# Performance work log

Hardware: AMD Instinct MI355X
Metric: run time of the kernel (lower is better)

## Reference

```python
import jax, jax.numpy as jnp
import numpy as np

B, S, E, H = 2, 2048, 1024, 16
D = E // H  # head_dim = 64


def setup_inputs() -> dict:
    key = jax.random.key(0)
    ks = jax.random.split(key, 6)
    scale = 1.0 / np.sqrt(E)
    query = jax.random.normal(ks[0], (B, S, E), dtype=jnp.float32)
    key_t = jax.random.normal(ks[1], (B, S, E), dtype=jnp.float32)
    # causal mask: True where future positions should be masked
    attention_mask = jnp.triu(jnp.ones((S, S), dtype=jnp.bool_), k=1)
    wq = jax.random.normal(ks[2], (E, E), dtype=jnp.float32) * scale
    wk = jax.random.normal(ks[3], (E, E), dtype=jnp.float32) * scale
    wv = jax.random.normal(ks[4], (E, E), dtype=jnp.float32) * scale
    wo = jax.random.normal(ks[5], (E, E), dtype=jnp.float32) * scale
    return {"query": query, "key": key_t, "attention_mask": attention_mask,
            "wq": wq, "wk": wk, "wv": wv, "wo": wo}


def _split_heads(x):
    # (B, S, E) -> (B, H, S, D)
    return x.reshape(B, S, H, D).transpose(0, 2, 1, 3)


def reference(query, key, attention_mask, wq, wk, wv, wo):
    # self-attention (encoder_decoder_attention=False): k, v from query
    q = _split_heads(query @ wq.T)
    k = _split_heads(query @ wk.T)
    v = _split_heads(query @ wv.T)
    scores = jnp.einsum('bhqd,bhkd->bhqk', q, k) / np.sqrt(D)
    # causal mask broadcast (1,1,S,S)
    scores = jnp.where(attention_mask[None, None, :, :], -jnp.inf, scores)
    attn_weights = jax.nn.softmax(scores, axis=-1)
    # drop_out = 0.0, so dropout is identity
    attn_out = jnp.einsum('bhqk,bhkd->bhqd', attn_weights, v)
    attn_out = attn_out.transpose(0, 2, 1, 3).reshape(B, S, E)
    attn_out = attn_out @ wo.T
    return attn_out, attn_weights
```

## Files before the change

kernel.cpp:

```cpp
#include <hip/hip_runtime.h>
#include <hip/hip_bf16.h>
#include <cstdint>

#define S_LEN 2048
#define EMB 1024
#define NHEAD 16
#define HDIM 64
#define NB 2
#define MTOT (NB * S_LEN)

typedef __attribute__((ext_vector_type(8))) __bf16 bf16x8;
typedef __attribute__((ext_vector_type(8))) unsigned short us8;
typedef __attribute__((ext_vector_type(4))) unsigned short us4;
typedef __attribute__((ext_vector_type(4))) float f32x4;

__device__ __forceinline__ unsigned short f2b(float f) {
  unsigned int u = __float_as_uint(f);
  u = (u + 0x7FFFu + ((u >> 16) & 1u)) >> 16;
  return (unsigned short)u;
}
__device__ __forceinline__ unsigned short f2b_tr(float f) {
  return (unsigned short)(__float_as_uint(f) >> 16);
}
__device__ __forceinline__ float b2f(unsigned short u) {
  return __uint_as_float((unsigned int)u << 16);
}
__device__ __forceinline__ bf16x8 ld8(const unsigned short* p) {
  return __builtin_bit_cast(bf16x8, *(const us8*)p);
}
__device__ __forceinline__ void gload16(const void* g, void* l) {
  __builtin_amdgcn_global_load_lds(
      (const __attribute__((address_space(1))) unsigned int*)g,
      (__attribute__((address_space(3))) unsigned int*)l, 16, 0, 0);
}
__device__ __forceinline__ void st_nt(float* p, f32x4 v) {
  __builtin_nontemporal_store(v, (f32x4*)p);
}
__device__ __forceinline__ void bar_lds() {
  asm volatile("s_waitcnt lgkmcnt(0)" ::: "memory");
  __builtin_amdgcn_sched_barrier(0);
  __builtin_amdgcn_s_barrier();
}
__device__ __forceinline__ void fence_lds_wave() {
  asm volatile("s_waitcnt lgkmcnt(0)" ::: "memory");
  __builtin_amdgcn_sched_barrier(0);
}

__global__ void conv_fused(const float* __restrict__ X,
                           const float* __restrict__ wq, const float* __restrict__ wk,
                           const float* __restrict__ wv, const float* __restrict__ wo,
                           unsigned short* __restrict__ xb,
                           unsigned short* __restrict__ wb) {
  int i = blockIdx.x * blockDim.x + threadIdx.x;
  const float* s;
  unsigned short* o;
  int j;
  float sc = 1.0f;
  if (i < MTOT * EMB / 4) {
    s = X; j = i; o = xb;
  } else {
    int k = i - MTOT * EMB / 4;
    int sel = k >> 18;
    j = k & 262143;
    s = sel == 0 ? wq : sel == 1 ? wk : sel == 2 ? wv : wo;
    o = wb + (size_t)sel * EMB * EMB;
    if (sel == 0) sc = 0.125f;
  }
  float4 v = reinterpret_cast<const float4*>(s)[j];
  us4 ov;
  ov[0] = f2b(v.x * sc); ov[1] = f2b(v.y * sc);
  ov[2] = f2b(v.z * sc); ov[3] = f2b(v.w * sc);
  reinterpret_cast<us4*>(o)[j] = ov;
}

__global__ __launch_bounds__(256)
void vtrans(const unsigned short* __restrict__ V, unsigned short* __restrict__ VT) {
  __shared__ unsigned short Vs[64][72];
  const int s0 = blockIdx.x * 64;
  const int bh = blockIdx.y, b = bh >> 4, h = bh & 15;
  const unsigned short* Vb = V + (size_t)b * S_LEN * EMB + h * HDIM;
  const int t = threadIdx.x;
  {
    int row = t >> 2, c0 = (t & 3) * 16;
    const unsigned short* src = Vb + (size_t)(s0 + row) * EMB + c0;
    *(us8*)&Vs[row][c0] = *(const us8*)src;
    *(us8*)&Vs[row][c0 + 8] = *(const us8*)(src + 8);
  }
  __syncthreads();
  int d = t >> 2, sc = (t & 3) * 16;
  us8 o0, o1;
#pragma unroll
  for (int j = 0; j < 8; ++j) { o0[j] = Vs[sc + j][d]; o1[j] = Vs[sc + 8 + j][d]; }
  unsigned short* dst = VT + ((size_t)bh * HDIM + d) * S_LEN + s0 + sc;
  *(us8*)dst = o0;
  *(us8*)(dst + 8) = o1;
}

template <typename OT>
__global__ __launch_bounds__(256)
void gemm_bt(const unsigned short* __restrict__ A,
             const unsigned short* __restrict__ Wb,
             OT* __restrict__ Cb) {
  __shared__ unsigned short As[128 * 32];
  __shared__ unsigned short Bs[128 * 32];
  const int t = threadIdx.x;
  const int w = t >> 6, l = t & 63;
  const int m0 = blockIdx.x * 128;
  const int n0g = blockIdx.y * 128;
  const int wsel = n0g >> 10;
  const int n0 = n0g & 1023;
  const unsigned short* W = Wb + (size_t)wsel * ((size_t)EMB * EMB);
  OT* C = Cb + (size_t)wsel * ((size_t)MTOT * EMB);
  const int wr = (w >> 1) * 64, wc = (w & 1) * 64;
  const int fr = l & 15, fk = (l >> 4) * 8;
  const f32x4 fz = {0.f, 0.f, 0.f, 0.f};
  f32x4 acc[4][4];
  for (int i = 0; i < 4; i++)
    for (int j = 0; j < 4; j++) acc[i][j] = fz;
  const int srow = t >> 2, scol = (t & 3) * 8;
  const unsigned short* Ar = A + (size_t)(m0 + srow) * EMB + scol;
  const unsigned short* Wr = W + (size_t)(n0 + srow) * EMB + scol;
  unsigned short* lA = &As[t * 8];
  unsigned short* lB = &Bs[t * 8];
  for (int k0 = 0; k0 < EMB; k0 += 32) {
    gload16(Ar + k0, lA);
    gload16(Ar + (size_t)64 * EMB + k0, lA + 64 * 32);
    gload16(Wr + k0, lB);
    gload16(Wr + (size_t)64 * EMB + k0, lB + 64 * 32);
    __syncthreads();
    bf16x8 af[4], bg[4];
#pragma unroll
    for (int i = 0; i < 4; i++) {
      af[i] = ld8(&As[(wr + i * 16 + fr) * 32 + fk]);
      bg[i] = ld8(&Bs[(wc + i * 16 + fr) * 32 + fk]);
    }
#pragma unroll
    for (int i = 0; i < 4; i++)
#pragma unroll
      for (int j = 0; j < 4; j++)
        acc[i][j] = __builtin_amdgcn_mfma_f32_16x16x32_bf16(af[i], bg[j], acc[i][j], 0, 0, 0);
    __syncthreads();
  }
  const int cr = (l >> 4) * 4, cc = l & 15;
#pragma unroll
  for (int i = 0; i < 4; i++)
#pragma unroll
    for (int j = 0; j < 4; j++) {
      int m = m0 + wr + i * 16 + cr;
      int n = n0 + wc + j * 16 + cc;
      OT* dst = C + (size_t)m * EMB + n;
#pragma unroll
      for (int r = 0; r < 4; r++) {
        if constexpr (sizeof(OT) == 2)
          dst[(size_t)r * EMB] = f2b(acc[i][j][r]);
        else
          __builtin_nontemporal_store(acc[i][j][r], dst + (size_t)r * EMB);
      }
    }
}

__global__ __launch_bounds__(256, 4)
void attn_fwd(const unsigned short* __restrict__ Q,
              const unsigned short* __restrict__ K,
              const unsigned short* __restrict__ VT,
              unsigned short* __restrict__ AO,
              float* __restrict__ WT) {
  __shared__ __align__(16) unsigned char smem[27648];
  unsigned short* Ks  = (unsigned short*)smem;
  unsigned short* Vt  = (unsigned short*)(smem + 9216);
  unsigned short* PsA = (unsigned short*)(smem + 18432);
  unsigned short* PsB = (unsigned short*)(smem + 23040);

  const int t = threadIdx.x, w = t >> 6, l = t & 63;
  const int p = blockIdx.x;
  const int bh = blockIdx.y, b = bh >> 4, h = bh & 15;
  const int z = blockIdx.z;
  const int qA = p, qB = 31 - p;
  const int ntA = p + 1, ntB = 32 - p;
  const int half = w >> 1;
  const int wrow = (w & 1) * 16;
  const int nt = half ? ntB : ntA;
  const int qbase = (half ? qB : qA) * 64 + z * 32;
  const unsigned short* Qb = Q + (size_t)b * S_LEN * EMB + h * HDIM;
  const unsigned short* Kb = K + (size_t)b * S_LEN * EMB + h * HDIM;
  const unsigned short* VTb = VT + (size_t)bh * HDIM * S_LEN;
  const int fr = l & 15, fk = (l >> 4) * 8;
  const int rg = (l >> 4) * 4;
  const int qrow = qbase + wrow + rg;
  const f32x4 fz = {0.f, 0.f, 0.f, 0.f};
  const int srow = t >> 3, scol = (t & 7) * 8;
  const int zrow = l >> 4, zcol = (l & 15) * 4;
  unsigned short* Psh = half ? PsB : PsA;

  {
    int row = t >> 3, c0 = (t & 7) * 8;
    *(us8*)&PsA[row * 72 + c0] =
        *(const us8*)(Qb + (size_t)(qA * 64 + z * 32 + row) * EMB + c0);
    *(us8*)&PsB[row * 72 + c0] =
        *(const us8*)(Qb + (size_t)(qB * 64 + z * 32 + row) * EMB + c0);
  }
  __syncthreads();
  bf16x8 qa0 = ld8(&Psh[(wrow + fr) * 72 + fk]);
  bf16x8 qa1 = ld8(&Psh[(wrow + fr) * 72 + 32 + fk]);

  float lr[4];
#pragma unroll
  for (int r = 0; r < 4; r++) lr[r] = 0.f;

  us8 k0r = *(const us8*)(Kb + (size_t)srow * EMB + scol);
  us8 k1r = *(const us8*)(Kb + (size_t)(srow + 32) * EMB + scol);
  for (int it = 0; it < ntB; ++it) {
    *(us8*)&Ks[srow * 72 + scol] = k0r;
    *(us8*)&Ks[(srow + 32) * 72 + scol] = k1r;
    us8 k0n, k1n;
    if (it + 1 < ntB) {
      const unsigned short* kn = Kb + (size_t)((it + 1) * 64) * EMB;
      k0n = *(const us8*)(kn + (size_t)srow * EMB + scol);
      k1n = *(const us8*)(kn + (size_t)(srow + 32) * EMB + scol);
    }
    bar_lds();
    const int kc = it * 64;
    if (it < nt) {
      const bool diag = (it == nt - 1);
#pragma unroll
      for (int c = 0; c < 4; ++c) {
        bf16x8 kb0 = ld8(&Ks[(c * 16 + fr) * 72 + fk]);
        bf16x8 kb1 = ld8(&Ks[(c * 16 + fr) * 72 + 32 + fk]);
        f32x4 dd = fz;
        dd = __builtin_amdgcn_mfma_f32_16x16x32_bf16(qa0, kb0, dd, 0, 0, 0);
        dd = __builtin_amdgcn_mfma_f32_16x16x32_bf16(qa1, kb1, dd, 0, 0, 0);
        int ki = kc + c * 16 + fr;
#pragma unroll
        for (int r = 0; r < 4; ++r) {
          float e = __expf(dd[r]);
          if (diag && ki > qrow + r) e = 0.f;
          lr[r] += e;
        }
      }
    } else {
#pragma unroll
      for (int s4 = 0; s4 < 4; ++s4) {
        int rowl = s4 * 4 + zrow;
        st_nt(&WT[((size_t)bh * S_LEN + qbase + wrow + rowl) * S_LEN + kc + zcol], fz);
      }
    }
    bar_lds();
    k0r = k0n; k1r = k1n;
  }
  for (int it = ntB; it < 32; ++it) {
    const int kc = it * 64;
#pragma unroll
    for (int s4 = 0; s4 < 4; ++s4) {
      int rowl = s4 * 4 + zrow;
      st_nt(&WT[((size_t)bh * S_LEN + qbase + wrow + rowl) * S_LEN + kc + zcol], fz);
    }
  }
#pragma unroll
  for (int r = 0; r < 4; ++r) {
    float v = lr[r];
    for (int s = 1; s < 16; s <<= 1) v += __shfl_xor(v, s, 64);
    lr[r] = 1.0f / v;
  }

  f32x4 acc[4];
#pragma unroll
  for (int i = 0; i < 4; i++) acc[i] = fz;
  us8 v0r, v1r;
  k0r = *(const us8*)(Kb + (size_t)srow * EMB + scol);
  k1r = *(const us8*)(Kb + (size_t)(srow + 32) * EMB + scol);
  v0r = *(const us8*)(VTb + (size_t)srow * S_LEN + scol);
  v1r = *(const us8*)(VTb + (size_t)(srow + 32) * S_LEN + scol);
  for (int it = 0; it < ntB; ++it) {
    *(us8*)&Ks[srow * 72 + scol] = k0r;
    *(us8*)&Ks[(srow + 32) * 72 + scol] = k1r;
    *(us8*)&Vt[srow * 72 + scol] = v0r;
    *(us8*)&Vt[(srow + 32) * 72 + scol] = v1r;
    us8 k0n, k1n, v0n, v1n;
    if (it + 1 < ntB) {
      const int kc1 = (it + 1) * 64;
      const unsigned short* kn = Kb + (size_t)kc1 * EMB;
      k0n = *(const us8*)(kn + (size_t)srow * EMB + scol);
      k1n = *(const us8*)(kn + (size_t)(srow + 32) * EMB + scol);
      v0n = *(const us8*)(VTb + (size_t)srow * S_LEN + kc1 + scol);
      v1n = *(const us8*)(VTb + (size_t)(srow + 32) * S_LEN + kc1 + scol);
    }
    bar_lds();
    const int kc = it * 64;
    if (it < nt) {
      const bool diag = (it == nt - 1);
#pragma unroll
      for (int c = 0; c < 4; ++c) {
        bf16x8 kb0 = ld8(&Ks[(c * 16 + fr) * 72 + fk]);
        bf16x8 kb1 = ld8(&Ks[(c * 16 + fr) * 72 + 32 + fk]);
        f32x4 dd = fz;
        dd = __builtin_amdgcn_mfma_f32_16x16x32_bf16(qa0, kb0, dd, 0, 0, 0);
        dd = __builtin_amdgcn_mfma_f32_16x16x32_bf16(qa1, kb1, dd, 0, 0, 0);
        int ki = kc + c * 16 + fr;
#pragma unroll
        for (int r = 0; r < 4; ++r) {
          float e = __expf(dd[r]);
          if (diag && ki > qrow + r) e = 0.f;
          Psh[(wrow + rg + r) * 72 + c * 16 + fr] = f2b_tr(e * lr[r]);
        }
      }
      fence_lds_wave();
#pragma unroll
      for (int ks = 0; ks < 2; ++ks) {
        bf16x8 pa = ld8(&Psh[(wrow + fr) * 72 + ks * 32 + fk]);
#pragma unroll
        for (int dt = 0; dt < 4; ++dt) {
          bf16x8 vb = ld8(&Vt[(dt * 16 + fr) * 72 + ks * 32 + fk]);
          acc[dt] = __builtin_amdgcn_mfma_f32_16x16x32_bf16(pa, vb, acc[dt], 0, 0, 0);
        }
      }
#pragma unroll
      for (int s4 = 0; s4 < 4; ++s4) {
        int rowl = s4 * 4 + zrow;
        us4 pv = *(const us4*)&Psh[(wrow + rowl) * 72 + zcol];
        f32x4 v;
#pragma unroll
        for (int j = 0; j < 4; ++j) v[j] = b2f(pv[j]);
        st_nt(&WT[((size_t)bh * S_LEN + qbase + wrow + rowl) * S_LEN + kc + zcol], v);
      }
    }
    bar_lds();
    k0r = k0n; k1r = k1n; v0r = v0n; v1r = v1n;
  }

#pragma unroll
  for (int dt = 0; dt < 4; ++dt)
#pragma unroll
    for (int r = 0; r < 4; ++r)
      Psh[(wrow + rg + r) * 72 + dt * 16 + fr] = f2b(acc[dt][r]);
  __syncthreads();
  {
    int orow = t >> 2;
    int oh = orow >> 5, orl = orow & 31;
    int d0 = (t & 3) * 16;
    const unsigned short* osrc =
        (const unsigned short*)(smem + 18432 + oh * 4608) + orl * 72 + d0;
    us8 o0 = *(const us8*)osrc;
    us8 o1 = *(const us8*)(osrc + 8);
    int grow = (oh ? qB : qA) * 64 + z * 32 + orl;
    unsigned short* dst = AO + (size_t)(b * S_LEN + grow) * EMB + h * HDIM + d0;
    *(us8*)dst = o0;
    *(us8*)(dst + 8) = o1;
  }
}

extern "C" void kernel_launch(void* const* d_in, const int* in_sizes, int n_in,
                              void* d_out, int out_size, void* d_ws, size_t ws_size,
                              hipStream_t stream) {
  const float* query = (const float*)d_in[0];
  const float* wq = (const float*)d_in[3];
  const float* wk = (const float*)d_in[4];
  const float* wv = (const float*)d_in[5];
  const float* wo = (const float*)d_in[6];

  float* out0 = (float*)d_out;
  float* wout = out0 + (size_t)MTOT * EMB;

  unsigned short* xb  = (unsigned short*)d_ws;
  unsigned short* wqb = xb + (size_t)MTOT * EMB;
  unsigned short* wob = wqb + (size_t)3 * EMB * EMB;
  unsigned short* qb  = wqb + (size_t)4 * EMB * EMB;
  unsigned short* kb  = qb + (size_t)MTOT * EMB;
  unsigned short* vb  = kb + (size_t)MTOT * EMB;
  unsigned short* ab  = vb + (size_t)MTOT * EMB;
  unsigned short* vtg = xb;

  conv_fused<<<dim3(8192), dim3(256), 0, stream>>>(query, wq, wk, wv, wo, xb, wqb);

  gemm_bt<unsigned short><<<dim3(MTOT / 128, 24), dim3(256), 0, stream>>>(xb, wqb, qb);

  vtrans<<<dim3(S_LEN / 64, NB * NHEAD), dim3(256), 0, stream>>>(vb, vtg);

  attn_fwd<<<dim3(16, NB * NHEAD, 2), dim3(256), 0, stream>>>(qb, kb, vtg, ab, wout);

  gemm_bt<float><<<dim3(MTOT / 128, 8), dim3(256), 0, stream>>>(ab, wob, out0);
}
```

Measured before the change: 245.7 us.

## Switch attention to single-wave blocks reading K/V directly from global memory

The attention kernel goes from 256-thread blocks with paired causal tiles and LDS-staged K/V tiles to 64-thread single-wave blocks, each handling 16 query rows. Blocks are scheduled heaviest-first by reversing the block index. K and V^T fragments are loaded straight from global memory into MFMA operands, which removes the block barriers and LDS staging. In exchange, K/V reuse across waves now depends on L1/L2 caching rather than shared memory, and global traffic and load latency per MFMA go up.

Result: slower. 430.9 us (+75.4%).

```diff
diff --git a/kernel.cpp b/kernel.cpp
--- a/kernel.cpp
+++ b/kernel.cpp
@@ -35,11 +35,6 @@
 }
 __device__ __forceinline__ void st_nt(float* p, f32x4 v) {
   __builtin_nontemporal_store(v, (f32x4*)p);
-}
-__device__ __forceinline__ void bar_lds() {
-  asm volatile("s_waitcnt lgkmcnt(0)" ::: "memory");
-  __builtin_amdgcn_sched_barrier(0);
-  __builtin_amdgcn_s_barrier();
 }
 __device__ __forceinline__ void fence_lds_wave() {
   asm volatile("s_waitcnt lgkmcnt(0)" ::: "memory");
@@ -159,100 +154,61 @@
     }
 }
 
-__global__ __launch_bounds__(256, 4)
+__global__ __launch_bounds__(64, 4)
 void attn_fwd(const unsigned short* __restrict__ Q,
               const unsigned short* __restrict__ K,
               const unsigned short* __restrict__ VT,
               unsigned short* __restrict__ AO,
               float* __restrict__ WT) {
-  __shared__ __align__(16) unsigned char smem[27648];
-  unsigned short* Ks  = (unsigned short*)smem;
-  unsigned short* Vt  = (unsigned short*)(smem + 9216);
-  unsigned short* PsA = (unsigned short*)(smem + 18432);
-  unsigned short* PsB = (unsigned short*)(smem + 23040);
-
-  const int t = threadIdx.x, w = t >> 6, l = t & 63;
-  const int p = blockIdx.x;
+  __shared__ __align__(16) unsigned short Ps[16 * 72];
+
+  const int l = threadIdx.x;
+  const int p16 = 127 - blockIdx.x;
   const int bh = blockIdx.y, b = bh >> 4, h = bh & 15;
-  const int z = blockIdx.z;
-  const int qA = p, qB = 31 - p;
-  const int ntA = p + 1, ntB = 32 - p;
-  const int half = w >> 1;
-  const int wrow = (w & 1) * 16;
-  const int nt = half ? ntB : ntA;
-  const int qbase = (half ? qB : qA) * 64 + z * 32;
+  const int nt = (p16 >> 2) + 1;
+  const int qbase = p16 * 16;
   const unsigned short* Qb = Q + (size_t)b * S_LEN * EMB + h * HDIM;
   const unsigned short* Kb = K + (size_t)b * S_LEN * EMB + h * HDIM;
   const unsigned short* VTb = VT + (size_t)bh * HDIM * S_LEN;
   const int fr = l & 15, fk = (l >> 4) * 8;
   const int rg = (l >> 4) * 4;
-  const int qrow = qbase + wrow + rg;
+  const int qrow = qbase + rg;
   const f32x4 fz = {0.f, 0.f, 0.f, 0.f};
-  const int srow = t >> 3, scol = (t & 7) * 8;
-  const int zrow = l >> 4, zcol = (l & 15) * 4;
-  unsigned short* Psh = half ? PsB : PsA;
-
-  {
-    int row = t >> 3, c0 = (t & 7) * 8;
-    *(us8*)&PsA[row * 72 + c0] =
-        *(const us8*)(Qb + (size_t)(qA * 64 + z * 32 + row) * EMB + c0);
-    *(us8*)&PsB[row * 72 + c0] =
-        *(const us8*)(Qb + (size_t)(qB * 64 + z * 32 + row) * EMB + c0);
-  }
-  __syncthreads();
-  bf16x8 qa0 = ld8(&Psh[(wrow + fr) * 72 + fk]);
-  bf16x8 qa1 = ld8(&Psh[(wrow + fr) * 72 + 32 + fk]);
+  const int zcol = (l & 15) * 4;
+
+  bf16x8 qa0 = ld8(Qb + (size_t)(qbase + fr) * EMB + fk);
+  bf16x8 qa1 = ld8(Qb + (size_t)(qbase + fr) * EMB + 32 + fk);
 
   float lr[4];
 #pragma unroll
   for (int r = 0; r < 4; r++) lr[r] = 0.f;
 
-  us8 k0r = *(const us8*)(Kb + (size_t)srow * EMB + scol);
-  us8 k1r = *(const us8*)(Kb + (size_t)(srow + 32) * EMB + scol);
-  for (int it = 0; it < ntB; ++it) {
-    *(us8*)&Ks[srow * 72 + scol] = k0r;
-    *(us8*)&Ks[(srow + 32) * 72 + scol] = k1r;
-    us8 k0n, k1n;
-    if (it + 1 < ntB) {
-      const unsigned short* kn = Kb + (size_t)((it + 1) * 64) * EMB;
-      k0n = *(const us8*)(kn + (size_t)srow * EMB + scol);
-      k1n = *(const us8*)(kn + (size_t)(srow + 32) * EMB + scol);
-    }
-    bar_lds();
+  for (int it = 0; it < nt; ++it) {
     const int kc = it * 64;
-    if (it < nt) {
-      const bool diag = (it == nt - 1);
-#pragma unroll
-      for (int c = 0; c < 4; ++c) {
-        bf16x8 kb0 = ld8(&Ks[(c * 16 + fr) * 72 + fk]);
-        bf16x8 kb1 = ld8(&Ks[(c * 16 + fr) * 72 + 32 + fk]);
-        f32x4 dd = fz;
-        dd = __builtin_amdgcn_mfma_f32_16x16x32_bf16(qa0, kb0, dd, 0, 0, 0);
-        dd = __builtin_amdgcn_mfma_f32_16x16x32_bf16(qa1, kb1, dd, 0, 0, 0);
-        int ki = kc + c * 16 + fr;
-#pragma unroll
-        for (int r = 0; r < 4; ++r) {
-          float e = __expf(dd[r]);
-          if (diag && ki > qrow + r) e = 0.f;
-          lr[r] += e;
-        }
+    const bool diag = (it == nt - 1);
+#pragma unroll
+    for (int c = 0; c < 4; ++c) {
+      const unsigned short* kr = Kb + (size_t)(kc + c * 16 + fr) * EMB;
+      bf16x8 kb0 = ld8(kr + fk);
+      bf16x8 kb1 = ld8(kr + 32 + fk);
+      f32x4 dd = fz;
+      dd = __builtin_amdgcn_mfma_f32_16x16x32_bf16(qa0, kb0, dd, 0, 0, 0);
+      dd = __builtin_amdgcn_mfma_f32_16x16x32_bf16(qa1, kb1, dd, 0, 0, 0);
+      int ki = kc + c * 16 + fr;
+#pragma unroll
+      for (int r = 0; r < 4; ++r) {
+        float e = __expf(dd[r]);
+        if (diag && ki > qrow + r) e = 0.f;
+        lr[r] += e;
       }
-    } else {
-#pragma unroll
-      for (int s4 = 0; s4 < 4; ++s4) {
-        int rowl = s4 * 4 + zrow;
-        st_nt(&WT[((size_t)bh * S_LEN + qbase + wrow + rowl) * S_LEN + kc + zcol], fz);
-      }
-    }
-    bar_lds();
-    k0r = k0n; k1r = k1n;
-  }
-  for (int it = ntB; it < 32; ++it) {
+    }
+  }
+  for (int it = nt; it < 32; ++it) {
     const int kc = it * 64;
 #pragma unroll
     for (int s4 = 0; s4 < 4; ++s4) {
-      int rowl = s4 * 4 + zrow;
-      st_nt(&WT[((size_t)bh * S_LEN + qbase + wrow + rowl) * S_LEN + kc + zcol], fz);
+      int rowl = s4 * 4 + (l >> 4);
+      st_nt(&WT[((size_t)bh * S_LEN + qbase + rowl) * S_LEN + kc + zcol], fz);
     }
   }
 #pragma unroll
@@ -265,84 +221,58 @@
   f32x4 acc[4];
 #pragma unroll
   for (int i = 0; i < 4; i++) acc[i] = fz;
-  us8 v0r, v1r;
-  k0r = *(const us8*)(Kb + (size_t)srow * EMB + scol);
-  k1r = *(const us8*)(Kb + (size_t)(srow + 32) * EMB + scol);
-  v0r = *(const us8*)(VTb + (size_t)srow * S_LEN + scol);
-  v1r = *(const us8*)(VTb + (size_t)(srow + 32) * S_LEN + scol);
-  for (int it = 0; it < ntB; ++it) {
-    *(us8*)&Ks[srow * 72 + scol] = k0r;
-    *(us8*)&Ks[(srow + 32) * 72 + scol] = k1r;
-    *(us8*)&Vt[srow * 72 + scol] = v0r;
-    *(us8*)&Vt[(srow + 32) * 72 + scol] = v1r;
-    us8 k0n, k1n, v0n, v1n;
-    if (it + 1 < ntB) {
-      const int kc1 = (it + 1) * 64;
-      const unsigned short* kn = Kb + (size_t)kc1 * EMB;
-      k0n = *(const us8*)(kn + (size_t)srow * EMB + scol);
-      k1n = *(const us8*)(kn + (size_t)(srow + 32) * EMB + scol);
-      v0n = *(const us8*)(VTb + (size_t)srow * S_LEN + kc1 + scol);
-      v1n = *(const us8*)(VTb + (size_t)(srow + 32) * S_LEN + kc1 + scol);
-    }
-    bar_lds();
+  for (int it = 0; it < nt; ++it) {
     const int kc = it * 64;
-    if (it < nt) {
-      const bool diag = (it == nt - 1);
-#pragma unroll
-      for (int c = 0; c < 4; ++c) {
-        bf16x8 kb0 = ld8(&Ks[(c * 16 + fr) * 72 + fk]);
-        bf16x8 kb1 = ld8(&Ks[(c * 16 + fr) * 72 + 32 + fk]);
-        f32x4 dd = fz;
-        dd = __builtin_amdgcn_mfma_f32_16x16x32_bf16(qa0, kb0, dd, 0, 0, 0);
-        dd = __builtin_amdgcn_mfma_f32_16x16x32_bf16(qa1, kb1, dd, 0, 0, 0);
-        int ki = kc + c * 16 + fr;
-#pragma unroll
-        for (int r = 0; r < 4; ++r) {
-          float e = __expf(dd[r]);
-          if (diag && ki > qrow + r) e = 0.f;
-          Psh[(wrow + rg + r) * 72 + c * 16 + fr] = f2b_tr(e * lr[r]);
-        }
+    const bool diag = (it == nt - 1);
+#pragma unroll
+    for (int c = 0; c < 4; ++c) {
+      const unsigned short* kr = Kb + (size_t)(kc + c * 16 + fr) * EMB;
+      bf16x8 kb0 = ld8(kr + fk);
+      bf16x8 kb1 = ld8(kr + 32 + fk);
+      f32x4 dd = fz;
+      dd = __builtin_amdgcn_mfma_f32_16x16x32_bf16(qa0, kb0, dd, 0, 0, 0);
+      dd = __builtin_amdgcn_mfma_f32_16x16x32_bf16(qa1, kb1, dd, 0, 0, 0);
+      int ki = kc + c * 16 + fr;
+#pragma unroll
+      for (int r = 0; r < 4; ++r) {
+        float e = __expf(dd[r]);
+        if (diag && ki > qrow + r) e = 0.f;
+        Ps[(rg + r) * 72 + c * 16 + fr] = f2b_tr(e * lr[r]);
       }
-      fence_lds_wave();
-#pragma unroll
-      for (int ks = 0; ks < 2; ++ks) {
-        bf16x8 pa = ld8(&Psh[(wrow + fr) * 72 + ks * 32 + fk]);
-#pragma unroll
-        for (int dt = 0; dt < 4; ++dt) {
-          bf16x8 vb = ld8(&Vt[(dt * 16 + fr) * 72 + ks * 32 + fk]);
-          acc[dt] = __builtin_amdgcn_mfma_f32_16x16x32_bf16(pa, vb, acc[dt], 0, 0, 0);
-        }
+    }
+    fence_lds_wave();
+#pragma unroll
+    for (int ks = 0; ks < 2; ++ks) {
+      bf16x8 pa = ld8(&Ps[fr * 72 + ks * 32 + fk]);
+#pragma unroll
+      for (int dt = 0; dt < 4; ++dt) {
+        bf16x8 vb = ld8(VTb + (size_t)(dt * 16 + fr) * S_LEN + kc + ks * 32 + fk);
+        acc[dt] = __builtin_amdgcn_mfma_f32_16x16x32_bf16(pa, vb, acc[dt], 0, 0, 0);
       }
-#pragma unroll
-      for (int s4 = 0; s4 < 4; ++s4) {
-        int rowl = s4 * 4 + zrow;
-        us4 pv = *(const us4*)&Psh[(wrow + rowl) * 72 + zcol];
-        f32x4 v;
-#pragma unroll
-        for (int j = 0; j < 4; ++j) v[j] = b2f(pv[j]);
-        st_nt(&WT[((size_t)bh * S_LEN + qbase + wrow + rowl) * S_LEN + kc + zcol], v);
-      }
-    }
-    bar_lds();
-    k0r = k0n; k1r = k1n; v0r = v0n; v1r = v1n;
+    }
+#pragma unroll
+    for (int s4 = 0; s4 < 4; ++s4) {
+      int rowl = s4 * 4 + (l >> 4);
+      us4 pv = *(const us4*)&Ps[rowl * 72 + zcol];
+      f32x4 v;
+#pragma unroll
+      for (int j = 0; j < 4; ++j) v[j] = b2f(pv[j]);
+      st_nt(&WT[((size_t)bh * S_LEN + qbase + rowl) * S_LEN + kc + zcol], v);
+    }
+    fence_lds_wave();
   }
 
 #pragma unroll
   for (int dt = 0; dt < 4; ++dt)
 #pragma unroll
     for (int r = 0; r < 4; ++r)
-      Psh[(wrow + rg + r) * 72 + dt * 16 + fr] = f2b(acc[dt][r]);
-  __syncthreads();
+      Ps[(rg + r) * 72 + dt * 16 + fr] = f2b(acc[dt][r]);
+  fence_lds_wave();
   {
-    int orow = t >> 2;
-    int oh = orow >> 5, orl = orow & 31;
-    int d0 = (t & 3) * 16;
-    const unsigned short* osrc =
-        (const unsigned short*)(smem + 18432 + oh * 4608) + orl * 72 + d0;
-    us8 o0 = *(const us8*)osrc;
-    us8 o1 = *(const us8*)(osrc + 8);
-    int grow = (oh ? qB : qA) * 64 + z * 32 + orl;
-    unsigned short* dst = AO + (size_t)(b * S_LEN + grow) * EMB + h * HDIM + d0;
+    int rowl = l >> 2, d0 = (l & 3) * 16;
+    us8 o0 = *(const us8*)&Ps[rowl * 72 + d0];
+    us8 o1 = *(const us8*)&Ps[rowl * 72 + d0 + 8];
+    unsigned short* dst = AO + (size_t)(b * S_LEN + qbase + rowl) * EMB + h * HDIM + d0;
     *(us8*)dst = o0;
     *(us8*)(dst + 8) = o1;
   }
@@ -375,7 +305,7 @@
 
   vtrans<<<dim3(S_LEN / 64, NB * NHEAD), dim3(256), 0, stream>>>(vb, vtg);
 
-  attn_fwd<<<dim3(16, NB * NHEAD, 2), dim3(256), 0, stream>>>(qb, kb, vtg, ab, wout);
+  attn_fwd<<<dim3(128, NB * NHEAD), dim3(64), 0, stream>>>(qb, kb, vtg, ab, wout);
 
   gemm_bt<float><<<dim3(MTOT / 128, 8), dim3(256), 0, stream>>>(ab, wob, out0);
 }
```

## Restructure attention: one 64-row q tile per block, fuse PV into first pass

Applied to the files above, without the earlier changes.

Each block now handles a single 64-row query tile, with heaviest tiles scheduled first, instead of pairing a light and a heavy half-tile per block. The first pass now computes unnormalized P·V along with the row sums, and normalization is applied to the output accumulator at the end. The second pass only recomputes the normalized weights for the attention-weights output and does not reload V. This drops the V loads and PV MFMAs from the second pass. In exchange it gives up the pairing-based load balance and leaves fewer, more uneven blocks.

After: 209.0 us. -14.9%, faster.

```diff
diff --git a/kernel.cpp b/kernel.cpp
--- a/kernel.cpp
+++ b/kernel.cpp
@@ -165,118 +165,56 @@
               const unsigned short* __restrict__ VT,
               unsigned short* __restrict__ AO,
               float* __restrict__ WT) {
-  __shared__ __align__(16) unsigned char smem[27648];
-  unsigned short* Ks  = (unsigned short*)smem;
-  unsigned short* Vt  = (unsigned short*)(smem + 9216);
-  unsigned short* PsA = (unsigned short*)(smem + 18432);
-  unsigned short* PsB = (unsigned short*)(smem + 23040);
+  __shared__ __align__(16) unsigned char smem[9216 * 3];
+  unsigned short* Ks = (unsigned short*)smem;
+  unsigned short* Vt = (unsigned short*)(smem + 9216);
+  unsigned short* Ps = (unsigned short*)(smem + 18432);
 
   const int t = threadIdx.x, w = t >> 6, l = t & 63;
-  const int p = blockIdx.x;
+  const int p = 31 - blockIdx.x;
   const int bh = blockIdx.y, b = bh >> 4, h = bh & 15;
-  const int z = blockIdx.z;
-  const int qA = p, qB = 31 - p;
-  const int ntA = p + 1, ntB = 32 - p;
-  const int half = w >> 1;
-  const int wrow = (w & 1) * 16;
-  const int nt = half ? ntB : ntA;
-  const int qbase = (half ? qB : qA) * 64 + z * 32;
+  const int nt = p + 1;
+  const int qbase = p * 64;
   const unsigned short* Qb = Q + (size_t)b * S_LEN * EMB + h * HDIM;
   const unsigned short* Kb = K + (size_t)b * S_LEN * EMB + h * HDIM;
   const unsigned short* VTb = VT + (size_t)bh * HDIM * S_LEN;
   const int fr = l & 15, fk = (l >> 4) * 8;
   const int rg = (l >> 4) * 4;
-  const int qrow = qbase + wrow + rg;
+  const int qrow = qbase + w * 16 + rg;
   const f32x4 fz = {0.f, 0.f, 0.f, 0.f};
   const int srow = t >> 3, scol = (t & 7) * 8;
   const int zrow = l >> 4, zcol = (l & 15) * 4;
-  unsigned short* Psh = half ? PsB : PsA;
+  unsigned short* Psw = Ps + w * (16 * 72);
 
   {
-    int row = t >> 3, c0 = (t & 7) * 8;
-    *(us8*)&PsA[row * 72 + c0] =
-        *(const us8*)(Qb + (size_t)(qA * 64 + z * 32 + row) * EMB + c0);
-    *(us8*)&PsB[row * 72 + c0] =
-        *(const us8*)(Qb + (size_t)(qB * 64 + z * 32 + row) * EMB + c0);
+    int row = t >> 2, c0 = (t & 3) * 16;
+    const unsigned short* src = Qb + (size_t)(qbase + row) * EMB + c0;
+    *(us8*)&Ps[row * 72 + c0] = *(const us8*)src;
+    *(us8*)&Ps[row * 72 + c0 + 8] = *(const us8*)(src + 8);
   }
   __syncthreads();
-  bf16x8 qa0 = ld8(&Psh[(wrow + fr) * 72 + fk]);
-  bf16x8 qa1 = ld8(&Psh[(wrow + fr) * 72 + 32 + fk]);
+  bf16x8 qa0 = ld8(&Ps[(w * 16 + fr) * 72 + fk]);
+  bf16x8 qa1 = ld8(&Ps[(w * 16 + fr) * 72 + 32 + fk]);
+  __syncthreads();
 
   float lr[4];
+  f32x4 acc[4];
 #pragma unroll
   for (int r = 0; r < 4; r++) lr[r] = 0.f;
+#pragma unroll
+  for (int i = 0; i < 4; i++) acc[i] = fz;
 
   us8 k0r = *(const us8*)(Kb + (size_t)srow * EMB + scol);
   us8 k1r = *(const us8*)(Kb + (size_t)(srow + 32) * EMB + scol);
-  for (int it = 0; it < ntB; ++it) {
-    *(us8*)&Ks[srow * 72 + scol] = k0r;
-    *(us8*)&Ks[(srow + 32) * 72 + scol] = k1r;
-    us8 k0n, k1n;
-    if (it + 1 < ntB) {
-      const unsigned short* kn = Kb + (size_t)((it + 1) * 64) * EMB;
-      k0n = *(const us8*)(kn + (size_t)srow * EMB + scol);
-      k1n = *(const us8*)(kn + (size_t)(srow + 32) * EMB + scol);
-    }
-    bar_lds();
-    const int kc = it * 64;
-    if (it < nt) {
-      const bool diag = (it == nt - 1);
-#pragma unroll
-      for (int c = 0; c < 4; ++c) {
-        bf16x8 kb0 = ld8(&Ks[(c * 16 + fr) * 72 + fk]);
-        bf16x8 kb1 = ld8(&Ks[(c * 16 + fr) * 72 + 32 + fk]);
-        f32x4 dd = fz;
-        dd = __builtin_amdgcn_mfma_f32_16x16x32_bf16(qa0, kb0, dd, 0, 0, 0);
-        dd = __builtin_amdgcn_mfma_f32_16x16x32_bf16(qa1, kb1, dd, 0, 0, 0);
-        int ki = kc + c * 16 + fr;
-#pragma unroll
-        for (int r = 0; r < 4; ++r) {
-          float e = __expf(dd[r]);
-          if (diag && ki > qrow + r) e = 0.f;
-          lr[r] += e;
-        }
-      }
-    } else {
-#pragma unroll
-      for (int s4 = 0; s4 < 4; ++s4) {
-        int rowl = s4 * 4 + zrow;
-        st_nt(&WT[((size_t)bh * S_LEN + qbase + wrow + rowl) * S_LEN + kc + zcol], fz);
-      }
-    }
-    bar_lds();
-    k0r = k0n; k1r = k1n;
-  }
-  for (int it = ntB; it < 32; ++it) {
-    const int kc = it * 64;
-#pragma unroll
-    for (int s4 = 0; s4 < 4; ++s4) {
-      int rowl = s4 * 4 + zrow;
-      st_nt(&WT[((size_t)bh * S_LEN + qbase + wrow + rowl) * S_LEN + kc + zcol], fz);
-    }
-  }
-#pragma unroll
-  for (int r = 0; r < 4; ++r) {
-    float v = lr[r];
-    for (int s = 1; s < 16; s <<= 1) v += __shfl_xor(v, s, 64);
-    lr[r] = 1.0f / v;
-  }
-
-  f32x4 acc[4];
-#pragma unroll
-  for (int i = 0; i < 4; i++) acc[i] = fz;
-  us8 v0r, v1r;
-  k0r = *(const us8*)(Kb + (size_t)srow * EMB + scol);
-  k1r = *(const us8*)(Kb + (size_t)(srow + 32) * EMB + scol);
-  v0r = *(const us8*)(VTb + (size_t)srow * S_LEN + scol);
-  v1r = *(const us8*)(VTb + (size_t)(srow + 32) * S_LEN + scol);
-  for (int it = 0; it < ntB; ++it) {
+  us8 v0r = *(const us8*)(VTb + (size_t)srow * S_LEN + scol);
+  us8 v1r = *(const us8*)(VTb + (size_t)(srow + 32) * S_LEN + scol);
+  for (int it = 0; it < nt; ++it) {
     *(us8*)&Ks[srow * 72 + scol] = k0r;
     *(us8*)&Ks[(srow + 32) * 72 + scol] = k1r;
     *(us8*)&Vt[srow * 72 + scol] = v0r;
     *(us8*)&Vt[(srow + 32) * 72 + scol] = v1r;
     us8 k0n, k1n, v0n, v1n;
-    if (it + 1 < ntB) {
+    if (it + 1 < nt) {
       const int kc1 = (it + 1) * 64;
       const unsigned short* kn = Kb + (size_t)kc1 * EMB;
       k0n = *(const us8*)(kn + (size_t)srow * EMB + scol);
@@ -286,63 +224,106 @@
     }
     bar_lds();
     const int kc = it * 64;
-    if (it < nt) {
-      const bool diag = (it == nt - 1);
-#pragma unroll
-      for (int c = 0; c < 4; ++c) {
-        bf16x8 kb0 = ld8(&Ks[(c * 16 + fr) * 72 + fk]);
-        bf16x8 kb1 = ld8(&Ks[(c * 16 + fr) * 72 + 32 + fk]);
-        f32x4 dd = fz;
-        dd = __builtin_amdgcn_mfma_f32_16x16x32_bf16(qa0, kb0, dd, 0, 0, 0);
-        dd = __builtin_amdgcn_mfma_f32_16x16x32_bf16(qa1, kb1, dd, 0, 0, 0);
-        int ki = kc + c * 16 + fr;
-#pragma unroll
-        for (int r = 0; r < 4; ++r) {
-          float e = __expf(dd[r]);
-          if (diag && ki > qrow + r) e = 0.f;
-          Psh[(wrow + rg + r) * 72 + c * 16 + fr] = f2b_tr(e * lr[r]);
-        }
+    const bool diag = (it == nt - 1);
+#pragma unroll
+    for (int c = 0; c < 4; ++c) {
+      bf16x8 kb0 = ld8(&Ks[(c * 16 + fr) * 72 + fk]);
+      bf16x8 kb1 = ld8(&Ks[(c * 16 + fr) * 72 + 32 + fk]);
+      f32x4 dd = fz;
+      dd = __builtin_amdgcn_mfma_f32_16x16x32_bf16(qa0, kb0, dd, 0, 0, 0);
+      dd = __builtin_amdgcn_mfma_f32_16x16x32_bf16(qa1, kb1, dd, 0, 0, 0);
+      int ki = kc + c * 16 + fr;
+#pragma unroll
+      for (int r = 0; r < 4; ++r) {
+        float e = __expf(dd[r]);
+        if (diag && ki > qrow + r) e = 0.f;
+        lr[r] += e;
+        Psw[(rg + r) * 72 + c * 16 + fr] = f2b_tr(e);
       }
-      fence_lds_wave();
-#pragma unroll
-      for (int ks = 0; ks < 2; ++ks) {
-        bf16x8 pa = ld8(&Psh[(wrow + fr) * 72 + ks * 32 + fk]);
-#pragma unroll
-        for (int dt = 0; dt < 4; ++dt) {
-          bf16x8 vb = ld8(&Vt[(dt * 16 + fr) * 72 + ks * 32 + fk]);
-          acc[dt] = __builtin_amdgcn_mfma_f32_16x16x32_bf16(pa, vb, acc[dt], 0, 0, 0);
-        }
-      }
-#pragma unroll
-      for (int s4 = 0; s4 < 4; ++s4) {
-        int rowl = s4 * 4 + zrow;
-        us4 pv = *(const us4*)&Psh[(wrow + rowl) * 72 + zcol];
-        f32x4 v;
-#pragma unroll
-        for (int j = 0; j < 4; ++j) v[j] = b2f(pv[j]);
-        st_nt(&WT[((size_t)bh * S_LEN + qbase + wrow + rowl) * S_LEN + kc + zcol], v);
+    }
+    fence_lds_wave();
+#pragma unroll
+    for (int ks = 0; ks < 2; ++ks) {
+      bf16x8 pa = ld8(&Psw[fr * 72 + ks * 32 + fk]);
+#pragma unroll
+      for (int dt = 0; dt < 4; ++dt) {
+        bf16x8 vb = ld8(&Vt[(dt * 16 + fr) * 72 + ks * 32 + fk]);
+        acc[dt] = __builtin_amdgcn_mfma_f32_16x16x32_bf16(pa, vb, acc[dt], 0, 0, 0);
       }
     }
     bar_lds();
     k0r = k0n; k1r = k1n; v0r = v0n; v1r = v1n;
   }
+  for (int it = nt; it < 32; ++it) {
+    const int kc = it * 64;
+#pragma unroll
+    for (int s4 = 0; s4 < 4; ++s4) {
+      int rowl = s4 * 4 + zrow;
+      st_nt(&WT[((size_t)bh * S_LEN + qbase + w * 16 + rowl) * S_LEN + kc + zcol], fz);
+    }
+  }
+#pragma unroll
+  for (int r = 0; r < 4; ++r) {
+    float v = lr[r];
+    for (int s = 1; s < 16; s <<= 1) v += __shfl_xor(v, s, 64);
+    lr[r] = 1.0f / v;
+  }
+
+  k0r = *(const us8*)(Kb + (size_t)srow * EMB + scol);
+  k1r = *(const us8*)(Kb + (size_t)(srow + 32) * EMB + scol);
+  for (int it = 0; it < nt; ++it) {
+    *(us8*)&Ks[srow * 72 + scol] = k0r;
+    *(us8*)&Ks[(srow + 32) * 72 + scol] = k1r;
+    us8 k0n, k1n;
+    if (it + 1 < nt) {
+      const unsigned short* kn = Kb + (size_t)((it + 1) * 64) * EMB;
+      k0n = *(const us8*)(kn + (size_t)srow * EMB + scol);
+      k1n = *(const us8*)(kn + (size_t)(srow + 32) * EMB + scol);
+    }
+    bar_lds();
+    const int kc = it * 64;
+    const bool diag = (it == nt - 1);
+#pragma unroll
+    for (int c = 0; c < 4; ++c) {
+      bf16x8 kb0 = ld8(&Ks[(c * 16 + fr) * 72 + fk]);
+      bf16x8 kb1 = ld8(&Ks[(c * 16 + fr) * 72 + 32 + fk]);
+      f32x4 dd = fz;
+      dd = __builtin_amdgcn_mfma_f32_16x16x32_bf16(qa0, kb0, dd, 0, 0, 0);
+      dd = __builtin_amdgcn_mfma_f32_16x16x32_bf16(qa1, kb1, dd, 0, 0, 0);
+      int ki = kc + c * 16 + fr;
+#pragma unroll
+      for (int r = 0; r < 4; ++r) {
+        float e = __expf(dd[r]);
+        if (diag && ki > qrow + r) e = 0.f;
+        Psw[(rg + r) * 72 + c * 16 + fr] = f2b_tr(e * lr[r]);
+      }
+    }
+    fence_lds_wave();
+#pragma unroll
+    for (int s4 = 0; s4 < 4; ++s4) {
+      int rowl = s4 * 4 + zrow;
+      us4 pv = *(const us4*)&Psw[rowl * 72 + zcol];
+      f32x4 v;
+#pragma unroll
+      for (int j = 0; j < 4; ++j) v[j] = b2f(pv[j]);
+      st_nt(&WT[((size_t)bh * S_LEN + qbase + w * 16 + rowl) * S_LEN + kc + zcol], v);
+    }
+    bar_lds();
+    k0r = k0n; k1r = k1n;
+  }
 
 #pragma unroll
   for (int dt = 0; dt < 4; ++dt)
 #pragma unroll
     for (int r = 0; r < 4; ++r)
-      Psh[(wrow + rg + r) * 72 + dt * 16 + fr] = f2b(acc[dt][r]);
+      Psw[(rg + r) * 72 + dt * 16 + fr] = f2b(acc[dt][r] * lr[r]);
   __syncthreads();
   {
-    int orow = t >> 2;
-    int oh = orow >> 5, orl = orow & 31;
-    int d0 = (t & 3) * 16;
-    const unsigned short* osrc =
-        (const unsigned short*)(smem + 18432 + oh * 4608) + orl * 72 + d0;
-    us8 o0 = *(const us8*)osrc;
-    us8 o1 = *(const us8*)(osrc + 8);
-    int grow = (oh ? qB : qA) * 64 + z * 32 + orl;
-    unsigned short* dst = AO + (size_t)(b * S_LEN + grow) * EMB + h * HDIM + d0;
+    int rowl = l >> 2, d0 = (l & 3) * 16;
+    us8 o0 = *(const us8*)&Ps[(w * 16 + rowl) * 72 + d0];
+    us8 o1 = *(const us8*)&Ps[(w * 16 + rowl) * 72 + d0 + 8];
+    unsigned short* dst =
+        AO + (size_t)(b * S_LEN + qbase + w * 16 + rowl) * EMB + h * HDIM + d0;
     *(us8*)dst = o0;
     *(us8*)(dst + 8) = o1;
   }
@@ -375,7 +356,7 @@
 
   vtrans<<<dim3(S_LEN / 64, NB * NHEAD), dim3(256), 0, stream>>>(vb, vtg);
 
-  attn_fwd<<<dim3(16, NB * NHEAD, 2), dim3(256), 0, stream>>>(qb, kb, vtg, ab, wout);
+  attn_fwd<<<dim3(32, NB * NHEAD), dim3(256), 0, stream>>>(qb, kb, vtg, ab, wout);
 
   gemm_bt<float><<<dim3(MTOT / 128, 8), dim3(256), 0, stream>>>(ab, wob, out0);
 }
```
